# Optimization experiments

Measured on AMD Instinct MI355X. Metric: run time of the kernel, lower is better.

## Reference

```python
import jax, jax.numpy as jnp
import numpy as np

D_MODEL = 1024
N_HEADS = 16
D_HIDDEN = 4096
BATCH = 2
N_CTX = 2048


def setup_inputs() -> dict:
    key = jax.random.key(0)
    ks = jax.random.split(key, 4)
    scale = 0.02
    x = jax.random.normal(ks[0], (BATCH, N_CTX, D_MODEL), dtype=jnp.float32)
    Wk = jax.random.normal(ks[1], (D_MODEL, D_MODEL), dtype=jnp.float32) * scale
    bk = jnp.zeros((D_MODEL,), dtype=jnp.float32)
    Wv = jax.random.normal(ks[2], (D_MODEL, D_HIDDEN), dtype=jnp.float32) * scale
    bv = jnp.zeros((D_HIDDEN,), dtype=jnp.float32)
    Wf = jax.random.normal(ks[3], (D_HIDDEN, D_MODEL), dtype=jnp.float32) * scale
    bf = jnp.zeros((D_MODEL,), dtype=jnp.float32)
    return {"x": x, "Wk": Wk, "bk": bk, "Wv": Wv, "bv": bv, "Wf": Wf, "bf": bf}


def _split_heads(t, n_heads):
    # [..., S, D] -> [..., H, S, D/H]
    B, S, D = t.shape
    return t.reshape(B, S, n_heads, D // n_heads).transpose(0, 2, 1, 3)


def reference(x, Wk, bk, Wv, bv, Wf, bf):
    B, S, D = x.shape
    H = N_HEADS
    # Q is raw x split into heads (no query projection in this module)
    Q = _split_heads(x, H)                  # [B,H,S,dk]
    K = _split_heads(x @ Wk + bk, H)        # [B,H,S,dk]
    V = _split_heads(x @ Wv + bv, H)        # [B,H,S,dv]
    # additive causal mask: 0 on/below diagonal, -inf strictly above
    causal = jnp.tril(jnp.ones((S, S), dtype=bool))
    mask = jnp.where(causal, 0.0, -jnp.inf).astype(x.dtype)
    # NOTE: no 1/sqrt(d) scaling, faithful to the original
    scores = jnp.einsum("bhqd,bhkd->bhqk", Q, K) + mask
    attn = jax.nn.softmax(scores, axis=-1)
    o = jnp.einsum("bhqk,bhkd->bhqd", attn, V)   # [B,H,S,dv]
    o = o.transpose(0, 2, 1, 3).reshape(B, S, -1)  # [B,S,d_hidden]
    return x + jax.nn.gelu(o, approximate=False) @ Wf + bf
```

## Files before the change

### kernel.cpp

```cpp
#include <hip/hip_runtime.h>
#include <math.h>

typedef unsigned short u16;
typedef __attribute__((ext_vector_type(8))) short bf16x8;
typedef __attribute__((ext_vector_type(4))) float f32x4;

__device__ __forceinline__ float b2f(u16 u) {
    union { unsigned int i; float f; } v; v.i = ((unsigned int)u) << 16; return v.f;
}
__device__ __forceinline__ u16 f2b(float f) {
    union { float f; unsigned int i; } v; v.f = f;
    unsigned int r = v.i + 0x7FFFu + ((v.i >> 16) & 1u);
    return (u16)(r >> 16);
}
__device__ __forceinline__ float gelu_exact(float v) {
    return 0.5f * v * (1.0f + erff(v * 0.70710678118654752f));
}

__device__ __forceinline__ void load_lds16(const u16* gp, u16* lp) {
    __builtin_amdgcn_global_load_lds(
        (const __attribute__((address_space(1))) void*)gp,
        (__attribute__((address_space(3))) void*)lp,
        16, 0, 0);
}

__global__ __launch_bounds__(256) void convert_f2b(const float* __restrict__ in,
                                                   u16* __restrict__ out) {
    const int idx = blockIdx.x * 256 + threadIdx.x;
    float4 v = ((const float4*)in)[idx];
    ushort4 u; u.x = f2b(v.x); u.y = f2b(v.y); u.z = f2b(v.z); u.w = f2b(v.w);
    ((ushort4*)out)[idx] = u;
}

__global__ __launch_bounds__(256) void transpose_w(const float* __restrict__ W,
                                                   u16* __restrict__ Wt, int N, int K) {
    __shared__ float t[32][33];
    const int tid = threadIdx.x;
    const int k0 = blockIdx.y * 32, n0 = blockIdx.x * 32;
    const int c = tid & 31, r = tid >> 5;
    #pragma unroll
    for (int p = 0; p < 4; p++)
        t[r + p * 8][c] = W[(size_t)(k0 + r + p * 8) * N + n0 + c];
    __syncthreads();
    #pragma unroll
    for (int p = 0; p < 4; p++)
        Wt[(size_t)(n0 + r + p * 8) * K + k0 + c] = f2b(t[c][r + p * 8]);
}

template <int EPI>
__global__ __launch_bounds__(256) void mfma_gemm(
    const u16* __restrict__ A, const u16* __restrict__ Bt,
    const float* __restrict__ bias, const float* __restrict__ resid,
    void* __restrict__ Cv, int M, int N, int K)
{
    __shared__ u16 As[64 * 64];
    __shared__ u16 Bs[128 * 64];

    const int tid = threadIdx.x;
    const int w = tid >> 6, lane = tid & 63;
    const int m16 = lane & 15, quad = lane >> 4;
    const int wm = w >> 1, wn = w & 1;
    const int row0 = blockIdx.y * 64, col0 = blockIdx.x * 128;
    const int lr = lane >> 3, lc = lane & 7;
    const int sw8 = (lc ^ (lr & 7)) * 8;

    f32x4 acc[2][4];
    #pragma unroll
    for (int i = 0; i < 2; i++)
        #pragma unroll
        for (int j = 0; j < 4; j++) acc[i][j] = (f32x4){0.f, 0.f, 0.f, 0.f};

    for (int k0 = 0; k0 < K; k0 += 64) {
        __syncthreads();
        #pragma unroll
        for (int c2 = 0; c2 < 2; c2++)
            load_lds16(A + (size_t)(row0 + c2 * 32 + w * 8 + lr) * K + k0 + sw8,
                       &As[(c2 * 32 + w * 8) * 64]);
        #pragma unroll
        for (int c2 = 0; c2 < 4; c2++)
            load_lds16(Bt + (size_t)(col0 + c2 * 32 + w * 8 + lr) * K + k0 + sw8,
                       &Bs[(c2 * 32 + w * 8) * 64]);
        __syncthreads();

        bf16x8 af[2][2], bfr[4][2];
        #pragma unroll
        for (int mt = 0; mt < 2; mt++)
            #pragma unroll
            for (int ks = 0; ks < 2; ks++)
                af[mt][ks] = *(const bf16x8*)&As[(wm * 32 + mt * 16 + m16) * 64 +
                                                 (((ks * 4 + quad) ^ (m16 & 7)) * 8)];
        #pragma unroll
        for (int nt = 0; nt < 4; nt++)
            #pragma unroll
            for (int ks = 0; ks < 2; ks++)
                bfr[nt][ks] = *(const bf16x8*)&Bs[(wn * 64 + nt * 16 + m16) * 64 +
                                                  (((ks * 4 + quad) ^ (m16 & 7)) * 8)];

        #pragma unroll
        for (int ks = 0; ks < 2; ks++)
            #pragma unroll
            for (int mt = 0; mt < 2; mt++)
                #pragma unroll
                for (int nt = 0; nt < 4; nt++)
                    acc[mt][nt] = __builtin_amdgcn_mfma_f32_16x16x32_bf16(af[mt][ks], bfr[nt][ks], acc[mt][nt], 0, 0, 0);
    }

    #pragma unroll
    for (int mt = 0; mt < 2; mt++) {
        #pragma unroll
        for (int nt = 0; nt < 4; nt++) {
            const int c = col0 + wn * 64 + nt * 16 + m16;
            const float bc = bias[c];
            if (EPI == 2) {
                const int r0 = row0 + wm * 32 + mt * 16 + quad * 4;
                const int bb = r0 >> 11, s = r0 & 2047;
                const int h = c >> 8, dv = c & 255;
                ushort4 w4;
                w4.x = f2b(acc[mt][nt][0] + bc);
                w4.y = f2b(acc[mt][nt][1] + bc);
                w4.z = f2b(acc[mt][nt][2] + bc);
                w4.w = f2b(acc[mt][nt][3] + bc);
                *(ushort4*)((u16*)Cv + (((size_t)((bb * 16 + h) * 256 + dv)) << 11) + s) = w4;
            } else {
                #pragma unroll
                for (int reg = 0; reg < 4; reg++) {
                    const int r = row0 + wm * 32 + mt * 16 + quad * 4 + reg;
                    float v = acc[mt][nt][reg] + bc;
                    if (EPI == 1) {
                        v += resid[(size_t)r * N + c];
                        ((float*)Cv)[(size_t)r * N + c] = v;
                    } else {
                        ((u16*)Cv)[(size_t)r * N + c] = f2b(v);
                    }
                }
            }
        }
    }
}

__global__ __launch_bounds__(256) void attn_kernel(
    const float* __restrict__ X,
    const u16*  __restrict__ Kb,
    const u16*  __restrict__ Vt,
    u16* __restrict__ O,
    int B, int S)
{
    const int DM = 1024, DH = 4096;
    __shared__ u16 Ks[64 * 64];
    __shared__ u16 Ps[64 * 64];
    __shared__ u16 Vts[256 * 64];

    const int tid = threadIdx.x;
    const int w = tid >> 6, lane = tid & 63;
    const int m16 = lane & 15, quad = lane >> 4;
    const int lr = lane >> 3, lc = lane & 7;
    const int sw8 = (lc ^ (lr & 7)) * 8;
    const int b = blockIdx.z, h = blockIdx.y;
    const int qt = (S / 64 - 1) - blockIdx.x;
    const int q0 = qt * 64;
    const size_t baseRow = (size_t)b * S;
    const size_t vhead = ((size_t)(b * 16 + h) * 256) << 11;

    bf16x8 aq[2];
    {
        const float* qsrc = X + (baseRow + q0 + w * 16 + m16) * DM + h * 64;
        #pragma unroll
        for (int ks = 0; ks < 2; ks++) {
            float4 v0 = *(const float4*)(qsrc + ks * 32 + quad * 8);
            float4 v1 = *(const float4*)(qsrc + ks * 32 + quad * 8 + 4);
            bf16x8 u;
            u[0] = (short)f2b(v0.x); u[1] = (short)f2b(v0.y); u[2] = (short)f2b(v0.z); u[3] = (short)f2b(v0.w);
            u[4] = (short)f2b(v1.x); u[5] = (short)f2b(v1.y); u[6] = (short)f2b(v1.z); u[7] = (short)f2b(v1.w);
            aq[ks] = u;
        }
    }

    f32x4 o_acc[16];
    #pragma unroll
    for (int i = 0; i < 16; i++) o_acc[i] = (f32x4){0.f, 0.f, 0.f, 0.f};
    f32x4 lacc = (f32x4){0.f, 0.f, 0.f, 0.f};

    bf16x8 onesf;
    {
        const short one = (m16 == 0) ? (short)0x3F80 : (short)0;
        #pragma unroll
        for (int i = 0; i < 8; i++) onesf[i] = one;
    }

    bf16x8 kreg[2], vreg[8];

    #pragma unroll
    for (int p = 0; p < 2; p++)
        kreg[p] = *(const bf16x8*)(Kb + (baseRow + p * 32 + w * 8 + lr) * DM + h * 64 + sw8);
    #pragma unroll
    for (int p = 0; p < 8; p++)
        vreg[p] = *(const bf16x8*)(Vt + vhead + (((size_t)(p * 32 + w * 8 + lr)) << 11) + sw8);
    #pragma unroll
    for (int p = 0; p < 2; p++)
        *(bf16x8*)&Ks[(p * 32 + w * 8) * 64 + lane * 8] = kreg[p];
    #pragma unroll
    for (int p = 0; p < 8; p++)
        *(bf16x8*)&Vts[(p * 32 + w * 8) * 64 + lane * 8] = vreg[p];
    __syncthreads();

    const int nch = qt + 1;
    for (int ch = 0; ch < nch; ch++) {
        const int k0 = ch * 64;

        if (ch + 1 < nch) {
            const int kn = k0 + 64;
            #pragma unroll
            for (int p = 0; p < 2; p++)
                kreg[p] = *(const bf16x8*)(Kb + (baseRow + kn + p * 32 + w * 8 + lr) * DM + h * 64 + sw8);
            #pragma unroll
            for (int p = 0; p < 8; p++)
                vreg[p] = *(const bf16x8*)(Vt + vhead + (((size_t)(p * 32 + w * 8 + lr)) << 11) + kn + sw8);
        }

        f32x4 sf[4];
        #pragma unroll
        for (int nt = 0; nt < 4; nt++) {
            f32x4 acc = (f32x4){0.f, 0.f, 0.f, 0.f};
            #pragma unroll
            for (int ks = 0; ks < 2; ks++) {
                bf16x8 bk8 = *(const bf16x8*)&Ks[(nt * 16 + m16) * 64 + (((ks * 4 + quad) ^ (m16 & 7)) * 8)];
                acc = __builtin_amdgcn_mfma_f32_16x16x32_bf16(aq[ks], bk8, acc, 0, 0, 0);
            }
            sf[nt] = acc;
        }

        const int qg = q0 + w * 16 + quad * 4;
        #pragma unroll
        for (int nt = 0; nt < 4; nt++) {
            const int kg = k0 + nt * 16 + m16;
            #pragma unroll
            for (int reg = 0; reg < 4; reg++) {
                const float p = (kg <= qg + reg) ? __expf(sf[nt][reg] - 20.f) : 0.f;
                const int srow = w * 16 + quad * 4 + reg;
                Ps[srow * 64 + (((nt * 2 + (m16 >> 3)) ^ (srow & 7)) * 8) + (m16 & 7)] = f2b(p);
            }
        }

        bf16x8 pa[2];
        #pragma unroll
        for (int ks = 0; ks < 2; ks++)
            pa[ks] = *(const bf16x8*)&Ps[(w * 16 + m16) * 64 + (((ks * 4 + quad) ^ (m16 & 7)) * 8)];
        #pragma unroll
        for (int ks = 0; ks < 2; ks++)
            lacc = __builtin_amdgcn_mfma_f32_16x16x32_bf16(pa[ks], onesf, lacc, 0, 0, 0);
        #pragma unroll
        for (int nt2 = 0; nt2 < 16; nt2++) {
            f32x4 acc = o_acc[nt2];
            #pragma unroll
            for (int ks = 0; ks < 2; ks++) {
                bf16x8 bv8 = *(const bf16x8*)&Vts[(nt2 * 16 + m16) * 64 + (((ks * 4 + quad) ^ (m16 & 7)) * 8)];
                acc = __builtin_amdgcn_mfma_f32_16x16x32_bf16(pa[ks], bv8, acc, 0, 0, 0);
            }
            o_acc[nt2] = acc;
        }

        __syncthreads();
        if (ch + 1 < nch) {
            #pragma unroll
            for (int p = 0; p < 2; p++)
                *(bf16x8*)&Ks[(p * 32 + w * 8) * 64 + lane * 8] = kreg[p];
            #pragma unroll
            for (int p = 0; p < 8; p++)
                *(bf16x8*)&Vts[(p * 32 + w * 8) * 64 + lane * 8] = vreg[p];
            __syncthreads();
        }
    }

    #pragma unroll
    for (int reg = 0; reg < 4; reg++) {
        const float l = __shfl(lacc[reg], quad * 16);
        const float invl = 1.0f / l;
        u16* orow = O + (baseRow + q0 + w * 16 + quad * 4 + reg) * DH + h * 256 + m16;
        #pragma unroll
        for (int nt2 = 0; nt2 < 16; nt2++)
            orow[nt2 * 16] = f2b(gelu_exact(o_acc[nt2][reg] * invl));
    }
}

extern "C" void kernel_launch(void* const* d_in, const int* in_sizes, int n_in,
                              void* d_out, int out_size, void* d_ws, size_t ws_size,
                              hipStream_t stream)
{
    const float* x   = (const float*)d_in[0];
    const float* Wk  = (const float*)d_in[1];
    const float* bk  = (const float*)d_in[2];
    const float* Wv  = (const float*)d_in[3];
    const float* bv  = (const float*)d_in[4];
    const float* Wf  = (const float*)d_in[5];
    const float* bfb = (const float*)d_in[6];
    float* out = (float*)d_out;

    const int Bsz = 2, S = 2048, DM = 1024, DH = 4096;
    const int M = Bsz * S;
    const size_t MB = 1024 * 1024;

    u16* xb   = (u16*)d_ws;
    u16* Wkt  = xb   + 4 * MB;
    u16* Wvt  = Wkt  + 1 * MB;
    u16* Wft  = Wvt  + 4 * MB;
    u16* Kbuf = Wft  + 4 * MB;
    u16* Vt   = Kbuf + 4 * MB;
    u16* Obuf = Vt   + 16 * MB;

    dim3 blk(256);

    convert_f2b<<<dim3(M * DM / 1024), blk, 0, stream>>>(x, xb);
    transpose_w<<<dim3(DM / 32, DM / 32), blk, 0, stream>>>(Wk, Wkt, DM, DM);
    transpose_w<<<dim3(DH / 32, DM / 32), blk, 0, stream>>>(Wv, Wvt, DH, DM);
    transpose_w<<<dim3(DM / 32, DH / 32), blk, 0, stream>>>(Wf, Wft, DM, DH);

    mfma_gemm<0><<<dim3(DM / 128, M / 64), blk, 0, stream>>>(xb, Wkt, bk, nullptr, Kbuf, M, DM, DM);
    mfma_gemm<2><<<dim3(DH / 128, M / 64), blk, 0, stream>>>(xb, Wvt, bv, nullptr, Vt, M, DH, DM);
    attn_kernel<<<dim3(S / 64, 16, Bsz), blk, 0, stream>>>(x, Kbuf, Vt, Obuf, Bsz, S);
    mfma_gemm<1><<<dim3(DM / 128, M / 64), blk, 0, stream>>>(Obuf, Wft, bfb, x, out, M, DM, DH);
}
```

Baseline: 388.7 us.

## Split attention PV work across waves by dv columns and enlarge V-projection GEMM tile

The attention kernel now gives each wave a 64-column slice of the 256-wide V head for all 64 query rows. V fragments are loaded straight from global memory into registers, so the V LDS tile and its staging go away, and P is shared through LDS. K prefetch is restructured to a single barrier-separated stage. Separately, the V projection uses a new 128x128-tile GEMM with the transposed-V epilogue, aiming for better operand reuse. Risks include uncoalesced V register loads, more sync points per chunk, and fewer blocks for the V GEMM.

```diff
diff --git a/kernel.cpp b/kernel.cpp
--- a/kernel.cpp
+++ b/kernel.cpp
@@ -111,29 +111,93 @@
         for (int nt = 0; nt < 4; nt++) {
             const int c = col0 + wn * 64 + nt * 16 + m16;
             const float bc = bias[c];
-            if (EPI == 2) {
-                const int r0 = row0 + wm * 32 + mt * 16 + quad * 4;
-                const int bb = r0 >> 11, s = r0 & 2047;
-                const int h = c >> 8, dv = c & 255;
-                ushort4 w4;
-                w4.x = f2b(acc[mt][nt][0] + bc);
-                w4.y = f2b(acc[mt][nt][1] + bc);
-                w4.z = f2b(acc[mt][nt][2] + bc);
-                w4.w = f2b(acc[mt][nt][3] + bc);
-                *(ushort4*)((u16*)Cv + (((size_t)((bb * 16 + h) * 256 + dv)) << 11) + s) = w4;
-            } else {
+            #pragma unroll
+            for (int reg = 0; reg < 4; reg++) {
+                const int r = row0 + wm * 32 + mt * 16 + quad * 4 + reg;
+                float v = acc[mt][nt][reg] + bc;
+                if (EPI == 1) {
+                    v += resid[(size_t)r * N + c];
+                    ((float*)Cv)[(size_t)r * N + c] = v;
+                } else {
+                    ((u16*)Cv)[(size_t)r * N + c] = f2b(v);
+                }
+            }
+        }
+    }
+}
+
+__global__ __launch_bounds__(256) void mfma_gemm128_tv(
+    const u16* __restrict__ A, const u16* __restrict__ Bt,
+    const float* __restrict__ bias,
+    u16* __restrict__ Cv, int M, int N, int K)
+{
+    __shared__ u16 As[128 * 64];
+    __shared__ u16 Bs[128 * 64];
+
+    const int tid = threadIdx.x;
+    const int w = tid >> 6, lane = tid & 63;
+    const int m16 = lane & 15, quad = lane >> 4;
+    const int wm = w >> 1, wn = w & 1;
+    const int row0 = blockIdx.y * 128, col0 = blockIdx.x * 128;
+    const int lr = lane >> 3, lc = lane & 7;
+    const int sw8 = (lc ^ (lr & 7)) * 8;
+
+    f32x4 acc[4][4];
+    #pragma unroll
+    for (int i = 0; i < 4; i++)
+        #pragma unroll
+        for (int j = 0; j < 4; j++) acc[i][j] = (f32x4){0.f, 0.f, 0.f, 0.f};
+
+    for (int k0 = 0; k0 < K; k0 += 64) {
+        __syncthreads();
+        #pragma unroll
+        for (int c2 = 0; c2 < 4; c2++)
+            load_lds16(A + (size_t)(row0 + c2 * 32 + w * 8 + lr) * K + k0 + sw8,
+                       &As[(c2 * 32 + w * 8) * 64]);
+        #pragma unroll
+        for (int c2 = 0; c2 < 4; c2++)
+            load_lds16(Bt + (size_t)(col0 + c2 * 32 + w * 8 + lr) * K + k0 + sw8,
+                       &Bs[(c2 * 32 + w * 8) * 64]);
+        __syncthreads();
+
+        bf16x8 af[4][2], bfr[4][2];
+        #pragma unroll
+        for (int mt = 0; mt < 4; mt++)
+            #pragma unroll
+            for (int ks = 0; ks < 2; ks++)
+                af[mt][ks] = *(const bf16x8*)&As[(wm * 64 + mt * 16 + m16) * 64 +
+                                                 (((ks * 4 + quad) ^ (m16 & 7)) * 8)];
+        #pragma unroll
+        for (int nt = 0; nt < 4; nt++)
+            #pragma unroll
+            for (int ks = 0; ks < 2; ks++)
+                bfr[nt][ks] = *(const bf16x8*)&Bs[(wn * 64 + nt * 16 + m16) * 64 +
+                                                  (((ks * 4 + quad) ^ (m16 & 7)) * 8)];
+
+        #pragma unroll
+        for (int ks = 0; ks < 2; ks++)
+            #pragma unroll
+            for (int mt = 0; mt < 4; mt++)
                 #pragma unroll
-                for (int reg = 0; reg < 4; reg++) {
-                    const int r = row0 + wm * 32 + mt * 16 + quad * 4 + reg;
-                    float v = acc[mt][nt][reg] + bc;
-                    if (EPI == 1) {
-                        v += resid[(size_t)r * N + c];
-                        ((float*)Cv)[(size_t)r * N + c] = v;
-                    } else {
-                        ((u16*)Cv)[(size_t)r * N + c] = f2b(v);
-                    }
-                }
-            }
+                for (int nt = 0; nt < 4; nt++)
+                    acc[mt][nt] = __builtin_amdgcn_mfma_f32_16x16x32_bf16(af[mt][ks], bfr[nt][ks], acc[mt][nt], 0, 0, 0);
+    }
+
+    #pragma unroll
+    for (int mt = 0; mt < 4; mt++) {
+        const int r0 = row0 + wm * 64 + mt * 16 + quad * 4;
+        const int bb = r0 >> 11, s = r0 & 2047;
+        #pragma unroll
+        for (int nt = 0; nt < 4; nt++) {
+            const int c = col0 + wn * 64 + nt * 16 + m16;
+            const int h = c >> 8, dv = c & 255;
+            const float bc = bias[c];
+            ushort4 w4;
+            w4.x = f2b(acc[mt][nt][0] + bc);
+            w4.y = f2b(acc[mt][nt][1] + bc);
+            w4.z = f2b(acc[mt][nt][2] + bc);
+            w4.w = f2b(acc[mt][nt][3] + bc);
+            *(ushort4*)(Cv + (((size_t)((bb * 16 + h) * 256 + dv)) << 11) + s) = w4;
         }
     }
 }
@@ -148,7 +212,6 @@
     const int DM = 1024, DH = 4096;
     __shared__ u16 Ks[64 * 64];
     __shared__ u16 Ps[64 * 64];
-    __shared__ u16 Vts[256 * 64];
 
     const int tid = threadIdx.x;
     const int w = tid >> 6, lane = tid & 63;
@@ -175,10 +238,14 @@
         }
     }
 
-    f32x4 o_acc[16];
-    #pragma unroll
-    for (int i = 0; i < 16; i++) o_acc[i] = (f32x4){0.f, 0.f, 0.f, 0.f};
-    f32x4 lacc = (f32x4){0.f, 0.f, 0.f, 0.f};
+    f32x4 o_acc[4][4];
+    #pragma unroll
+    for (int i = 0; i < 4; i++)
+        #pragma unroll
+        for (int j = 0; j < 4; j++) o_acc[i][j] = (f32x4){0.f, 0.f, 0.f, 0.f};
+    f32x4 lacc4[4];
+    #pragma unroll
+    for (int i = 0; i < 4; i++) lacc4[i] = (f32x4){0.f, 0.f, 0.f, 0.f};
 
     bf16x8 onesf;
     {
@@ -187,37 +254,32 @@
         for (int i = 0; i < 8; i++) onesf[i] = one;
     }
 
-    bf16x8 kreg[2], vreg[8];
+    bf16x8 kreg[2], vreg[4][2];
+    const int nch = qt + 1;
 
     #pragma unroll
     for (int p = 0; p < 2; p++)
         kreg[p] = *(const bf16x8*)(Kb + (baseRow + p * 32 + w * 8 + lr) * DM + h * 64 + sw8);
     #pragma unroll
-    for (int p = 0; p < 8; p++)
-        vreg[p] = *(const bf16x8*)(Vt + vhead + (((size_t)(p * 32 + w * 8 + lr)) << 11) + sw8);
+    for (int nt2 = 0; nt2 < 4; nt2++)
+        #pragma unroll
+        for (int ks = 0; ks < 2; ks++)
+            vreg[nt2][ks] = *(const bf16x8*)(Vt + vhead +
+                (((size_t)(w * 64 + nt2 * 16 + m16)) << 11) + ks * 32 + quad * 8);
     #pragma unroll
     for (int p = 0; p < 2; p++)
         *(bf16x8*)&Ks[(p * 32 + w * 8) * 64 + lane * 8] = kreg[p];
-    #pragma unroll
-    for (int p = 0; p < 8; p++)
-        *(bf16x8*)&Vts[(p * 32 + w * 8) * 64 + lane * 8] = vreg[p];
+    if (nch > 1) {
+        #pragma unroll
+        for (int p = 0; p < 2; p++)
+            kreg[p] = *(const bf16x8*)(Kb + (baseRow + 64 + p * 32 + w * 8 + lr) * DM + h * 64 + sw8);
+    }
     __syncthreads();
 
-    const int nch = qt + 1;
     for (int ch = 0; ch < nch; ch++) {
         const int k0 = ch * 64;
 
-        if (ch + 1 < nch) {
-            const int kn = k0 + 64;
-            #pragma unroll
-            for (int p = 0; p < 2; p++)
-                kreg[p] = *(const bf16x8*)(Kb + (baseRow + kn + p * 32 + w * 8 + lr) * DM + h * 64 + sw8);
-            #pragma unroll
-            for (int p = 0; p < 8; p++)
-                vreg[p] = *(const bf16x8*)(Vt + vhead + (((size_t)(p * 32 + w * 8 + lr)) << 11) + kn + sw8);
-        }
-
-        f32x4 sf[4];
+        const int qg = q0 + w * 16 + quad * 4;
         #pragma unroll
         for (int nt = 0; nt < 4; nt++) {
             f32x4 acc = (f32x4){0.f, 0.f, 0.f, 0.f};
@@ -226,59 +288,64 @@
                 bf16x8 bk8 = *(const bf16x8*)&Ks[(nt * 16 + m16) * 64 + (((ks * 4 + quad) ^ (m16 & 7)) * 8)];
                 acc = __builtin_amdgcn_mfma_f32_16x16x32_bf16(aq[ks], bk8, acc, 0, 0, 0);
             }
-            sf[nt] = acc;
-        }
-
-        const int qg = q0 + w * 16 + quad * 4;
-        #pragma unroll
-        for (int nt = 0; nt < 4; nt++) {
             const int kg = k0 + nt * 16 + m16;
             #pragma unroll
             for (int reg = 0; reg < 4; reg++) {
-                const float p = (kg <= qg + reg) ? __expf(sf[nt][reg] - 20.f) : 0.f;
+                const float p = (kg <= qg + reg) ? __expf(acc[reg] - 20.f) : 0.f;
                 const int srow = w * 16 + quad * 4 + reg;
                 Ps[srow * 64 + (((nt * 2 + (m16 >> 3)) ^ (srow & 7)) * 8) + (m16 & 7)] = f2b(p);
             }
         }
-
-        bf16x8 pa[2];
-        #pragma unroll
-        for (int ks = 0; ks < 2; ks++)
-            pa[ks] = *(const bf16x8*)&Ps[(w * 16 + m16) * 64 + (((ks * 4 + quad) ^ (m16 & 7)) * 8)];
-        #pragma unroll
-        for (int ks = 0; ks < 2; ks++)
-            lacc = __builtin_amdgcn_mfma_f32_16x16x32_bf16(pa[ks], onesf, lacc, 0, 0, 0);
-        #pragma unroll
-        for (int nt2 = 0; nt2 < 16; nt2++) {
-            f32x4 acc = o_acc[nt2];
-            #pragma unroll
-            for (int ks = 0; ks < 2; ks++) {
-                bf16x8 bv8 = *(const bf16x8*)&Vts[(nt2 * 16 + m16) * 64 + (((ks * 4 + quad) ^ (m16 & 7)) * 8)];
-                acc = __builtin_amdgcn_mfma_f32_16x16x32_bf16(pa[ks], bv8, acc, 0, 0, 0);
-            }
-            o_acc[nt2] = acc;
-        }
-
-        __syncthreads();
+        __syncthreads();
+
         if (ch + 1 < nch) {
             #pragma unroll
             for (int p = 0; p < 2; p++)
                 *(bf16x8*)&Ks[(p * 32 + w * 8) * 64 + lane * 8] = kreg[p];
-            #pragma unroll
-            for (int p = 0; p < 8; p++)
-                *(bf16x8*)&Vts[(p * 32 + w * 8) * 64 + lane * 8] = vreg[p];
-            __syncthreads();
-        }
-    }
-
-    #pragma unroll
-    for (int reg = 0; reg < 4; reg++) {
-        const float l = __shfl(lacc[reg], quad * 16);
-        const float invl = 1.0f / l;
-        u16* orow = O + (baseRow + q0 + w * 16 + quad * 4 + reg) * DH + h * 256 + m16;
-        #pragma unroll
-        for (int nt2 = 0; nt2 < 16; nt2++)
-            orow[nt2 * 16] = f2b(gelu_exact(o_acc[nt2][reg] * invl));
+            if (ch + 2 < nch) {
+                #pragma unroll
+                for (int p = 0; p < 2; p++)
+                    kreg[p] = *(const bf16x8*)(Kb + (baseRow + k0 + 128 + p * 32 + w * 8 + lr) * DM + h * 64 + sw8);
+            }
+        }
+
+        #pragma unroll
+        for (int mt = 0; mt < 4; mt++) {
+            bf16x8 pa0 = *(const bf16x8*)&Ps[(mt * 16 + m16) * 64 + (((0 + quad) ^ (m16 & 7)) * 8)];
+            bf16x8 pa1 = *(const bf16x8*)&Ps[(mt * 16 + m16) * 64 + (((4 + quad) ^ (m16 & 7)) * 8)];
+            lacc4[mt] = __builtin_amdgcn_mfma_f32_16x16x32_bf16(pa0, onesf, lacc4[mt], 0, 0, 0);
+            lacc4[mt] = __builtin_amdgcn_mfma_f32_16x16x32_bf16(pa1, onesf, lacc4[mt], 0, 0, 0);
+            #pragma unroll
+            for (int nt2 = 0; nt2 < 4; nt2++) {
+                f32x4 acc = o_acc[mt][nt2];
+                acc = __builtin_amdgcn_mfma_f32_16x16x32_bf16(pa0, vreg[nt2][0], acc, 0, 0, 0);
+                acc = __builtin_amdgcn_mfma_f32_16x16x32_bf16(pa1, vreg[nt2][1], acc, 0, 0, 0);
+                o_acc[mt][nt2] = acc;
+            }
+        }
+
+        if (ch + 1 < nch) {
+            #pragma unroll
+            for (int nt2 = 0; nt2 < 4; nt2++)
+                #pragma unroll
+                for (int ks = 0; ks < 2; ks++)
+                    vreg[nt2][ks] = *(const bf16x8*)(Vt + vhead +
+                        (((size_t)(w * 64 + nt2 * 16 + m16)) << 11) + (k0 + 64) + ks * 32 + quad * 8);
+        }
+        __syncthreads();
+    }
+
+    #pragma unroll
+    for (int mt = 0; mt < 4; mt++) {
+        #pragma unroll
+        for (int reg = 0; reg < 4; reg++) {
+            const float l = __shfl(lacc4[mt][reg], quad * 16);
+            const float invl = 1.0f / l;
+            u16* orow = O + (baseRow + q0 + mt * 16 + quad * 4 + reg) * DH + h * 256 + w * 64 + m16;
+            #pragma unroll
+            for (int nt2 = 0; nt2 < 4; nt2++)
+                orow[nt2 * 16] = f2b(gelu_exact(o_acc[mt][nt2][reg] * invl));
+        }
     }
 }
 
@@ -315,7 +382,7 @@
     transpose_w<<<dim3(DM / 32, DH / 32), blk, 0, stream>>>(Wf, Wft, DM, DH);
 
     mfma_gemm<0><<<dim3(DM / 128, M / 64), blk, 0, stream>>>(xb, Wkt, bk, nullptr, Kbuf, M, DM, DM);
-    mfma_gemm<2><<<dim3(DH / 128, M / 64), blk, 0, stream>>>(xb, Wvt, bv, nullptr, Vt, M, DH, DM);
+    mfma_gemm128_tv<<<dim3(DH / 128, M / 128), blk, 0, stream>>>(xb, Wvt, bv, Vt, M, DH, DM);
     attn_kernel<<<dim3(S / 64, 16, Bsz), blk, 0, stream>>>(x, Kbuf, Vt, Obuf, Bsz, S);
     mfma_gemm<1><<<dim3(DM / 128, M / 64), blk, 0, stream>>>(Obuf, Wft, bfb, x, out, M, DM, DH);
 }
```

After: 400.9 us. +3.1%, slower.
